# Performance work log

Hardware: AMD Instinct MI355X
Metric: run time of the kernel (lower is better)

The kernel has to match this reference:

```python
import jax, jax.numpy as jnp
import numpy as np

EMB = 1024
HEADS = 16
HEAD_DIM = EMB // HEADS


def setup_inputs() -> dict:
    key = jax.random.key(0)
    ks = jax.random.split(key, 6)
    B, T, D = 4, 2048, EMB
    s = 1.0 / np.sqrt(D)
    return {
        "x": jax.random.normal(ks[0], (B, T, D), dtype=jnp.float32),
        "Wq": jax.random.normal(ks[1], (D, D), dtype=jnp.float32) * s,
        "Wk": jax.random.normal(ks[2], (D, D), dtype=jnp.float32) * s,
        "Wv": jax.random.normal(ks[3], (D, D), dtype=jnp.float32) * s,
        "Wo": jax.random.normal(ks[4], (D, D), dtype=jnp.float32) * s,
        "bo": jax.random.normal(ks[5], (D,), dtype=jnp.float32) * 0.01,
    }


def reference(x, Wq, Wk, Wv, Wo, bo):
    B, T, D = x.shape
    H, Hd = HEADS, HEAD_DIM
    # torch Linear: x @ W.T ; here W stored [out,in]
    def heads(W):
        return (x @ W.T).reshape(B, T, H, Hd).transpose(0, 2, 1, 3)  # [B,H,T,Hd]
    Q, K, V = heads(Wq), heads(Wk), heads(Wv)
    scores = jnp.einsum("bhqd,bhkd->bhqk", Q, K) / np.sqrt(Hd)
    causal = jnp.triu(jnp.ones((T, T), dtype=bool), k=1)
    scores = jnp.where(causal, -jnp.inf, scores)
    weights = jax.nn.softmax(scores, axis=-1)  # dropout rate 0 -> identity
    ctx = jnp.einsum("bhqk,bhkd->bhqd", weights, V)
    ctx = ctx.transpose(0, 2, 1, 3).reshape(B, T, D)
    return ctx @ Wo.T + bo
```

## Files before the change

kernel.cpp:

```cpp
#include <hip/hip_runtime.h>

typedef short bf16x8 __attribute__((ext_vector_type(8)));
typedef float f32x4 __attribute__((ext_vector_type(4)));
typedef unsigned short u16;
typedef unsigned int u32;

__device__ __forceinline__ u16 f2b(float x) {
  union { float f; u32 u; } c; c.f = x;
  u32 r = (c.u + 0x7FFFu + ((c.u >> 16) & 1u)) >> 16;
  return (u16)r;
}

__device__ __forceinline__ float fexp2(float x) {
  return __builtin_amdgcn_exp2f(x);
}

__device__ __forceinline__ void glds16(const void* g, void* l) {
  __builtin_amdgcn_global_load_lds(
      (const __attribute__((address_space(1))) u32*)g,
      (__attribute__((address_space(3))) u32*)l, 16, 0, 0);
}

__global__ void cvt_kernel(const float* __restrict__ src, u16* __restrict__ dst,
                           int n4, float scale) {
  int i = blockIdx.x * blockDim.x + threadIdx.x;
  if (i >= n4) return;
  float4 v = reinterpret_cast<const float4*>(src)[i];
  ushort4 o;
  o.x = f2b(v.x * scale); o.y = f2b(v.y * scale);
  o.z = f2b(v.z * scale); o.w = f2b(v.w * scale);
  reinterpret_cast<ushort4*>(dst)[i] = o;
}

template<int MODE>
__global__ __launch_bounds__(512, 2)
void gemm2(const u16* __restrict__ A, const u16* __restrict__ Bm,
           u16* __restrict__ Cq, u16* __restrict__ Ck, u16* __restrict__ Cvt,
           float* __restrict__ Cf, const float* __restrict__ bias) {
  constexpr int K = 1024, NKT = K / 64;
  __shared__ __attribute__((aligned(16))) u16 lds[3][24576];
  const int tid = threadIdx.x;
  const int w = tid >> 6;
  const int l = tid & 63;
  const int wm = w >> 2, wn = w & 3;
  const int lr = l & 15, lg = l >> 4;
  const int brow = blockIdx.x * 128;
  const int bcol = blockIdx.y * 256;
  const int wg = w * 64;

  const u16* Ab = A + (size_t)brow * K;
  const u16* Bb = Bm + (size_t)bcol * K;
  int gA[2], lA[2], gB[4], lB[4];
#pragma unroll
  for (int i = 0; i < 2; ++i) {
    const int q = i * 512 + tid;
    const int r = q >> 3, s = (q & 7) ^ (r & 7);
    gA[i] = r * K + s * 8;
    lA[i] = (i * 512 + wg) * 8;
  }
#pragma unroll
  for (int i = 0; i < 4; ++i) {
    const int q = i * 512 + tid;
    const int r = q >> 3, s = (q & 7) ^ (r & 7);
    gB[i] = r * K + s * 8;
    lB[i] = 8192 + (i * 512 + wg) * 8;
  }

  int aoff[4][2], boff[4][2];
#pragma unroll
  for (int m = 0; m < 4; ++m) {
    const int row = wm * 64 + m * 16 + lr;
#pragma unroll
    for (int kk = 0; kk < 2; ++kk)
      aoff[m][kk] = row * 64 + (((kk * 4 + lg) ^ (row & 7)) * 8);
  }
#pragma unroll
  for (int n = 0; n < 4; ++n) {
    const int row = wn * 64 + n * 16 + lr;
#pragma unroll
    for (int kk = 0; kk < 2; ++kk)
      boff[n][kk] = 8192 + row * 64 + (((kk * 4 + lg) ^ (row & 7)) * 8);
  }

  f32x4 acc[4][4] = {};

#pragma unroll
  for (int i = 0; i < 2; ++i) glds16(Ab + gA[i], &lds[0][lA[i]]);
#pragma unroll
  for (int i = 0; i < 4; ++i) glds16(Bb + gB[i], &lds[0][lB[i]]);
#pragma unroll
  for (int i = 0; i < 2; ++i) glds16(Ab + gA[i] + 64, &lds[1][lA[i]]);
#pragma unroll
  for (int i = 0; i < 4; ++i) glds16(Bb + gB[i] + 64, &lds[1][lB[i]]);
  asm volatile("s_waitcnt vmcnt(6)" ::: "memory");
  asm volatile("s_barrier" ::: "memory");

  int bi = 0;
  for (int kt = 0; kt < NKT; ++kt) {
    const u16* Lb = lds[bi];
    const int bs = (bi + 2 >= 3) ? (bi - 1) : (bi + 2);
    const bool st = (kt + 2 < NKT);
    const int ko = (kt + 2) * 64;

    bf16x8 a[4][2], b01[2][2];
#pragma unroll
    for (int m = 0; m < 4; ++m)
#pragma unroll
      for (int kk = 0; kk < 2; ++kk)
        a[m][kk] = *reinterpret_cast<const bf16x8*>(&Lb[aoff[m][kk]]);
#pragma unroll
    for (int n = 0; n < 2; ++n)
#pragma unroll
      for (int kk = 0; kk < 2; ++kk)
        b01[n][kk] = *reinterpret_cast<const bf16x8*>(&Lb[boff[n][kk]]);
    if (st) {
      glds16(Ab + gA[0] + ko, &lds[bs][lA[0]]);
      glds16(Ab + gA[1] + ko, &lds[bs][lA[1]]);
      glds16(Bb + gB[0] + ko, &lds[bs][lB[0]]);
    }
    asm volatile("s_barrier" ::: "memory");
    asm volatile("s_waitcnt lgkmcnt(0)" ::: "memory");
    __builtin_amdgcn_sched_barrier(0);
    __builtin_amdgcn_s_setprio(1);
#pragma unroll
    for (int m = 0; m < 4; ++m)
#pragma unroll
      for (int n = 0; n < 2; ++n)
#pragma unroll
        for (int kk = 0; kk < 2; ++kk)
          acc[m][n] = __builtin_amdgcn_mfma_f32_16x16x32_bf16(a[m][kk], b01[n][kk], acc[m][n], 0, 0, 0);
    __builtin_amdgcn_s_setprio(0);
    asm volatile("s_barrier" ::: "memory");

    bf16x8 b23[2][2];
#pragma unroll
    for (int n = 0; n < 2; ++n)
#pragma unroll
      for (int kk = 0; kk < 2; ++kk)
        b23[n][kk] = *reinterpret_cast<const bf16x8*>(&Lb[boff[n + 2][kk]]);
    if (st) {
      glds16(Bb + gB[1] + ko, &lds[bs][lB[1]]);
      glds16(Bb + gB[2] + ko, &lds[bs][lB[2]]);
      glds16(Bb + gB[3] + ko, &lds[bs][lB[3]]);
    }
    if (kt + 1 < NKT) {
      if (st) asm volatile("s_waitcnt vmcnt(6)" ::: "memory");
      else    asm volatile("s_waitcnt vmcnt(0)" ::: "memory");
    }
    asm volatile("s_barrier" ::: "memory");
    asm volatile("s_waitcnt lgkmcnt(0)" ::: "memory");
    __builtin_amdgcn_sched_barrier(0);
    __builtin_amdgcn_s_setprio(1);
#pragma unroll
    for (int m = 0; m < 4; ++m)
#pragma unroll
      for (int n = 0; n < 2; ++n)
#pragma unroll
        for (int kk = 0; kk < 2; ++kk)
          acc[m][n + 2] = __builtin_amdgcn_mfma_f32_16x16x32_bf16(a[m][kk], b23[n][kk], acc[m][n + 2], 0, 0, 0);
    __builtin_amdgcn_s_setprio(0);
    asm volatile("s_barrier" ::: "memory");

    bi = (bi + 1 >= 3) ? 0 : bi + 1;
  }

  if (MODE == 0) {
    const int seg = blockIdx.y >> 2;
    const int cbase = (blockIdx.y & 3) * 256;
    if (seg < 2) {
      u16* dst = (seg == 0) ? Cq : Ck;
#pragma unroll
      for (int m = 0; m < 4; ++m) {
        const size_t r = (size_t)(brow + wm * 64 + m * 16 + lg * 4);
#pragma unroll
        for (int n = 0; n < 4; ++n) {
          const int c = cbase + wn * 64 + n * 16 + lr;
#pragma unroll
          for (int j = 0; j < 4; ++j)
            dst[(r + j) * 1024 + c] = f2b(acc[m][n][j]);
        }
      }
    } else {
#pragma unroll
      for (int n = 0; n < 4; ++n) {
        const int c = cbase + wn * 64 + n * 16 + lr;
        const int hh = c >> 6, dd = c & 63;
#pragma unroll
        for (int m = 0; m < 4; ++m) {
          const int r0 = brow + wm * 64 + m * 16 + lg * 4;
#pragma unroll
          for (int j = 0; j < 4; ++j) {
            const int r = r0 + j;
            const int bt = r >> 11, tt = r & 2047;
            Cvt[((size_t)((bt * 16 + hh) * 64 + dd)) * 2048 + tt] = f2b(acc[m][n][j]);
          }
        }
      }
    }
  } else {
#pragma unroll
    for (int m = 0; m < 4; ++m) {
      const size_t r = (size_t)(brow + wm * 64 + m * 16 + lg * 4);
#pragma unroll
      for (int n = 0; n < 4; ++n) {
        const int c = bcol + wn * 64 + n * 16 + lr;
        const float bv = bias[c];
#pragma unroll
        for (int j = 0; j < 4; ++j)
          Cf[(r + j) * 1024 + c] = acc[m][n][j] + bv;
      }
    }
  }
}

__global__ __launch_bounds__(256, 3)
void attn_kernel(const u16* __restrict__ qb, const u16* __restrict__ kb,
                 const u16* __restrict__ vt, u16* __restrict__ ctx) {
  __shared__ __attribute__((aligned(16))) u16 Ks[2][64 * 72];
  __shared__ __attribute__((aligned(16))) u16 Vs[2][64 * 72];
  __shared__ __attribute__((aligned(16))) u16 Ps[4 * 32 * 64];
  const int bid = blockIdx.x;
  const int qt = 15 - (bid >> 6);
  const int bh = bid & 63;
  const int bb = bh >> 4, h = bh & 15;
  const int tid = threadIdx.x, w = tid >> 6, l = tid & 63;
  const int lr = l & 15, lg = l >> 4;
  const int Qw = qt * 128 + w * 32;
  const int kvr = tid >> 3;
  const int kvc = (tid & 7) * 8;

  bf16x8 qf[2][2];
#pragma unroll
  for (int mi = 0; mi < 2; ++mi)
#pragma unroll
    for (int kc = 0; kc < 2; ++kc)
      qf[mi][kc] = *reinterpret_cast<const bf16x8*>(
          &qb[(size_t)(bb * 2048 + Qw + mi * 16 + lr) * 1024 + h * 64 + kc * 32 + lg * 8]);

  f32x4 oacc[2][4] = {};
  float lsum[2][4] = {};

  const int ntiles = 2 * qt + 2;

  bf16x8 kr[2], vr[2];
#pragma unroll
  for (int it = 0; it < 2; ++it) {
    kr[it] = *reinterpret_cast<const bf16x8*>(
        &kb[(size_t)(bb * 2048 + it * 32 + kvr) * 1024 + h * 64 + kvc]);
    vr[it] = *reinterpret_cast<const bf16x8*>(
        &vt[(size_t)(bh * 64 + it * 32 + kvr) * 2048 + kvc]);
  }
#pragma unroll
  for (int it = 0; it < 2; ++it) {
    *reinterpret_cast<bf16x8*>(&Ks[0][(it * 32 + kvr) * 72 + kvc]) = kr[it];
    *reinterpret_cast<bf16x8*>(&Vs[0][(it * 32 + kvr) * 72 + kvc]) = vr[it];
  }
  __syncthreads();
#pragma unroll
  for (int it = 0; it < 2; ++it) {
    kr[it] = *reinterpret_cast<const bf16x8*>(
        &kb[(size_t)(bb * 2048 + 64 + it * 32 + kvr) * 1024 + h * 64 + kvc]);
    vr[it] = *reinterpret_cast<const bf16x8*>(
        &vt[(size_t)(bh * 64 + it * 32 + kvr) * 2048 + 64 + kvc]);
  }

  for (int t = 0; t < ntiles; ++t) {
    const int c0 = t * 64;
    const int cur = t & 1;

    if (c0 < Qw + 32) {
      const bool diag = (c0 + 63 > Qw);

      f32x4 sacc[2][4] = {};
      __builtin_amdgcn_s_setprio(1);
#pragma unroll
      for (int kc = 0; kc < 2; ++kc)
#pragma unroll
        for (int nj = 0; nj < 4; ++nj) {
          bf16x8 kf = *reinterpret_cast<const bf16x8*>(
              &Ks[cur][(nj * 16 + lr) * 72 + kc * 32 + lg * 8]);
#pragma unroll
          for (int mi = 0; mi < 2; ++mi)
            sacc[mi][nj] = __builtin_amdgcn_mfma_f32_16x16x32_bf16(qf[mi][kc], kf, sacc[mi][nj], 0, 0, 0);
        }
      __builtin_amdgcn_s_setprio(0);

#pragma unroll
      for (int mi = 0; mi < 2; ++mi) {
        if (diag) {
#pragma unroll
          for (int nj = 0; nj < 4; ++nj) {
            const int col = c0 + nj * 16 + lr;
#pragma unroll
            for (int j = 0; j < 4; ++j) {
              const int row = Qw + mi * 16 + lg * 4 + j;
              if (col > row) sacc[mi][nj][j] = -1e30f;
            }
          }
        }
#pragma unroll
        for (int nj = 0; nj < 4; ++nj) {
          const int cchunk = nj * 2 + (lr >> 3);
          const int coff = lr & 7;
#pragma unroll
          for (int j = 0; j < 4; ++j) {
            const float p = fexp2(sacc[mi][nj][j]);
            lsum[mi][j] += p;
            const int rowP = mi * 16 + lg * 4 + j;
            Ps[w * 2048 + rowP * 64 + ((cchunk ^ (rowP & 7)) * 8) + coff] = f2b(p);
          }
        }
      }

      __builtin_amdgcn_s_setprio(1);
#pragma unroll
      for (int kc = 0; kc < 2; ++kc) {
        bf16x8 pf[2];
#pragma unroll
        for (int mi = 0; mi < 2; ++mi) {
          const int rowP = mi * 16 + lr;
          const int cj = kc * 4 + lg;
          pf[mi] = *reinterpret_cast<const bf16x8*>(
              &Ps[w * 2048 + rowP * 64 + ((cj ^ (rowP & 7)) * 8)]);
        }
#pragma unroll
        for (int nd = 0; nd < 4; ++nd) {
          bf16x8 vf = *reinterpret_cast<const bf16x8*>(
              &Vs[cur][(nd * 16 + lr) * 72 + kc * 32 + lg * 8]);
#pragma unroll
          for (int mi = 0; mi < 2; ++mi)
            oacc[mi][nd] = __builtin_amdgcn_mfma_f32_16x16x32_bf16(pf[mi], vf, oacc[mi][nd], 0, 0, 0);
        }
      }
      __builtin_amdgcn_s_setprio(0);
    }

    if (t + 1 < ntiles) {
#pragma unroll
      for (int it = 0; it < 2; ++it) {
        *reinterpret_cast<bf16x8*>(&Ks[cur ^ 1][(it * 32 + kvr) * 72 + kvc]) = kr[it];
        *reinterpret_cast<bf16x8*>(&Vs[cur ^ 1][(it * 32 + kvr) * 72 + kvc]) = vr[it];
      }
    }
    __syncthreads();
    if (t + 2 < ntiles) {
      const int c0n = c0 + 128;
#pragma unroll
      for (int it = 0; it < 2; ++it) {
        kr[it] = *reinterpret_cast<const bf16x8*>(
            &kb[(size_t)(bb * 2048 + c0n + it * 32 + kvr) * 1024 + h * 64 + kvc]);
        vr[it] = *reinterpret_cast<const bf16x8*>(
            &vt[(size_t)(bh * 64 + it * 32 + kvr) * 2048 + c0n + kvc]);
      }
    }
  }

#pragma unroll
  for (int mi = 0; mi < 2; ++mi) {
#pragma unroll
    for (int x = 1; x < 16; x <<= 1)
#pragma unroll
      for (int j = 0; j < 4; ++j) lsum[mi][j] += __shfl_xor(lsum[mi][j], x, 64);
#pragma unroll
    for (int j = 0; j < 4; ++j) {
      const float inv = 1.0f / lsum[mi][j];
      const size_t r = (size_t)(bb * 2048 + Qw + mi * 16 + lg * 4 + j);
#pragma unroll
      for (int nd = 0; nd < 4; ++nd)
        ctx[r * 1024 + h * 64 + nd * 16 + lr] = f2b(oacc[mi][nd][j] * inv);
    }
  }
}

extern "C" void kernel_launch(void* const* d_in, const int* in_sizes, int n_in,
                              void* d_out, int out_size, void* d_ws, size_t ws_size,
                              hipStream_t stream) {
  const float* x = (const float*)d_in[0];
  const float* Wq = (const float*)d_in[1];
  const float* Wk = (const float*)d_in[2];
  const float* Wv = (const float*)d_in[3];
  const float* Wo = (const float*)d_in[4];
  const float* bo = (const float*)d_in[5];
  float* out = (float*)d_out;

  char* ws = (char*)d_ws;
  u16* xb = (u16*)(ws);
  u16* qb = (u16*)(ws + (16u << 20));
  u16* kb = (u16*)(ws + (32u << 20));
  u16* vtb = (u16*)(ws + (64u << 20));
  u16* wqkvb = (u16*)(ws + (80u << 20));
  u16* wob = (u16*)(ws + (88u << 20));

  const float qscale = 0.125f * 1.4426950408889634f;
  cvt_kernel<<<8192, 256, 0, stream>>>(x, xb, 8388608 / 4, 1.0f);
  cvt_kernel<<<1024, 256, 0, stream>>>(Wq, wqkvb, 1048576 / 4, qscale);
  cvt_kernel<<<1024, 256, 0, stream>>>(Wk, wqkvb + 1048576, 1048576 / 4, 1.0f);
  cvt_kernel<<<1024, 256, 0, stream>>>(Wv, wqkvb + 2097152, 1048576 / 4, 1.0f);
  cvt_kernel<<<1024, 256, 0, stream>>>(Wo, wob, 1048576 / 4, 1.0f);

  gemm2<0><<<dim3(64, 12), 512, 0, stream>>>(xb, wqkvb, qb, kb, vtb, nullptr, nullptr);
  attn_kernel<<<1024, 256, 0, stream>>>(qb, kb, vtb, xb);
  gemm2<1><<<dim3(64, 4), 512, 0, stream>>>(xb, wob, nullptr, nullptr, nullptr, out, bo);
}
```

Measured before the change: 166.4 us.

## Restructure GEMM to 4 waves with 64x128 warp tiles and fuse conversion kernels

The projection GEMMs now run 256-thread blocks with 4 waves, each owning a 64x128 output sub-tile (32 accumulators). The K-step shrinks to 32 with a 3-stage LDS ring using a 4-way XOR swizzle, and the split half-iteration barrier scheme is dropped. The five fp32-to-bf16 conversion launches are merged into one kernel that selects source and scale by index. This aims for more register-level reuse per LDS read and fewer launches, at the cost of higher register pressure, twice as many loop iterations, and fewer waves to hide latency.

```diff
diff --git a/kernel.cpp b/kernel.cpp
--- a/kernel.cpp
+++ b/kernel.cpp
@@ -21,146 +21,114 @@
       (__attribute__((address_space(3))) u32*)l, 16, 0, 0);
 }
 
-__global__ void cvt_kernel(const float* __restrict__ src, u16* __restrict__ dst,
-                           int n4, float scale) {
-  int i = blockIdx.x * blockDim.x + threadIdx.x;
-  if (i >= n4) return;
-  float4 v = reinterpret_cast<const float4*>(src)[i];
+__global__ void cvt_all(const float* __restrict__ x, const float* __restrict__ Wq,
+                        const float* __restrict__ Wk, const float* __restrict__ Wv,
+                        const float* __restrict__ Wo, u16* __restrict__ xb,
+                        u16* __restrict__ wqkvb, u16* __restrict__ wob, float qscale) {
+  const int i = blockIdx.x * blockDim.x + threadIdx.x;
+  const float* src;
+  u16* dst;
+  float scale = 1.0f;
+  int off;
+  if (i < 2097152) {
+    src = x; dst = xb; off = i;
+  } else {
+    const int j = i - 2097152;
+    const int wsel = j >> 18;
+    off = j & 262143;
+    if (wsel == 0)      { src = Wq; dst = wqkvb;            scale = qscale; }
+    else if (wsel == 1) { src = Wk; dst = wqkvb + 1048576; }
+    else if (wsel == 2) { src = Wv; dst = wqkvb + 2097152; }
+    else                { src = Wo; dst = wob; }
+  }
+  float4 v = reinterpret_cast<const float4*>(src)[off];
   ushort4 o;
   o.x = f2b(v.x * scale); o.y = f2b(v.y * scale);
   o.z = f2b(v.z * scale); o.w = f2b(v.w * scale);
-  reinterpret_cast<ushort4*>(dst)[i] = o;
+  reinterpret_cast<ushort4*>(dst)[off] = o;
 }
 
 template<int MODE>
-__global__ __launch_bounds__(512, 2)
+__global__ __launch_bounds__(256, 2)
 void gemm2(const u16* __restrict__ A, const u16* __restrict__ Bm,
            u16* __restrict__ Cq, u16* __restrict__ Ck, u16* __restrict__ Cvt,
            float* __restrict__ Cf, const float* __restrict__ bias) {
-  constexpr int K = 1024, NKT = K / 64;
-  __shared__ __attribute__((aligned(16))) u16 lds[3][24576];
+  constexpr int K = 1024, NKT = 32;
+  __shared__ __attribute__((aligned(16))) u16 lds[3][12288];
   const int tid = threadIdx.x;
-  const int w = tid >> 6;
-  const int l = tid & 63;
-  const int wm = w >> 2, wn = w & 3;
+  const int w = tid >> 6, l = tid & 63;
+  const int wm = w >> 1, wn = w & 1;
   const int lr = l & 15, lg = l >> 4;
   const int brow = blockIdx.x * 128;
   const int bcol = blockIdx.y * 256;
-  const int wg = w * 64;
-
   const u16* Ab = A + (size_t)brow * K;
   const u16* Bb = Bm + (size_t)bcol * K;
-  int gA[2], lA[2], gB[4], lB[4];
+
+  int gA[2], gB[4];
 #pragma unroll
   for (int i = 0; i < 2; ++i) {
-    const int q = i * 512 + tid;
-    const int r = q >> 3, s = (q & 7) ^ (r & 7);
-    gA[i] = r * K + s * 8;
-    lA[i] = (i * 512 + wg) * 8;
+    const int q = i * 256 + tid, r = q >> 2, s = q & 3;
+    gA[i] = r * K + ((s ^ (r & 3)) * 8);
   }
 #pragma unroll
   for (int i = 0; i < 4; ++i) {
-    const int q = i * 512 + tid;
-    const int r = q >> 3, s = (q & 7) ^ (r & 7);
-    gB[i] = r * K + s * 8;
-    lB[i] = 8192 + (i * 512 + wg) * 8;
-  }
-
-  int aoff[4][2], boff[4][2];
+    const int q = i * 256 + tid, r = q >> 2, s = q & 3;
+    gB[i] = r * K + ((s ^ (r & 3)) * 8);
+  }
+  const int ldsw = w * 512;
+
+  int a_off[4], b_off[8];
 #pragma unroll
   for (int m = 0; m < 4; ++m) {
     const int row = wm * 64 + m * 16 + lr;
-#pragma unroll
-    for (int kk = 0; kk < 2; ++kk)
-      aoff[m][kk] = row * 64 + (((kk * 4 + lg) ^ (row & 7)) * 8);
-  }
-#pragma unroll
-  for (int n = 0; n < 4; ++n) {
-    const int row = wn * 64 + n * 16 + lr;
-#pragma unroll
-    for (int kk = 0; kk < 2; ++kk)
-      boff[n][kk] = 8192 + row * 64 + (((kk * 4 + lg) ^ (row & 7)) * 8);
-  }
-
-  f32x4 acc[4][4] = {};
-
-#pragma unroll
-  for (int i = 0; i < 2; ++i) glds16(Ab + gA[i], &lds[0][lA[i]]);
-#pragma unroll
-  for (int i = 0; i < 4; ++i) glds16(Bb + gB[i], &lds[0][lB[i]]);
-#pragma unroll
-  for (int i = 0; i < 2; ++i) glds16(Ab + gA[i] + 64, &lds[1][lA[i]]);
-#pragma unroll
-  for (int i = 0; i < 4; ++i) glds16(Bb + gB[i] + 64, &lds[1][lB[i]]);
+    a_off[m] = (row * 4 + (lg ^ (lr & 3))) * 8;
+  }
+#pragma unroll
+  for (int n = 0; n < 8; ++n) {
+    const int row = wn * 128 + n * 16 + lr;
+    b_off[n] = 4096 + (row * 4 + (lg ^ (lr & 3))) * 8;
+  }
+
+  f32x4 acc[4][8] = {};
+
+#pragma unroll
+  for (int t = 0; t < 2; ++t) {
+#pragma unroll
+    for (int i = 0; i < 2; ++i) glds16(Ab + gA[i] + t * 32, &lds[t][i * 2048 + ldsw]);
+#pragma unroll
+    for (int i = 0; i < 4; ++i) glds16(Bb + gB[i] + t * 32, &lds[t][4096 + i * 2048 + ldsw]);
+  }
   asm volatile("s_waitcnt vmcnt(6)" ::: "memory");
   asm volatile("s_barrier" ::: "memory");
 
   int bi = 0;
   for (int kt = 0; kt < NKT; ++kt) {
     const u16* Lb = lds[bi];
-    const int bs = (bi + 2 >= 3) ? (bi - 1) : (bi + 2);
-    const bool st = (kt + 2 < NKT);
-    const int ko = (kt + 2) * 64;
-
-    bf16x8 a[4][2], b01[2][2];
+    bf16x8 a[4], b[8];
+#pragma unroll
+    for (int m = 0; m < 4; ++m) a[m] = *reinterpret_cast<const bf16x8*>(&Lb[a_off[m]]);
+#pragma unroll
+    for (int n = 0; n < 8; ++n) b[n] = *reinterpret_cast<const bf16x8*>(&Lb[b_off[n]]);
+    if (kt + 2 < NKT) {
+      const int bs = (bi + 2 >= 3) ? (bi - 1) : (bi + 2);
+      const int ko = (kt + 2) * 32;
+#pragma unroll
+      for (int i = 0; i < 2; ++i) glds16(Ab + gA[i] + ko, &lds[bs][i * 2048 + ldsw]);
+#pragma unroll
+      for (int i = 0; i < 4; ++i) glds16(Bb + gB[i] + ko, &lds[bs][4096 + i * 2048 + ldsw]);
+    }
+    __builtin_amdgcn_s_setprio(1);
 #pragma unroll
     for (int m = 0; m < 4; ++m)
 #pragma unroll
-      for (int kk = 0; kk < 2; ++kk)
-        a[m][kk] = *reinterpret_cast<const bf16x8*>(&Lb[aoff[m][kk]]);
-#pragma unroll
-    for (int n = 0; n < 2; ++n)
-#pragma unroll
-      for (int kk = 0; kk < 2; ++kk)
-        b01[n][kk] = *reinterpret_cast<const bf16x8*>(&Lb[boff[n][kk]]);
-    if (st) {
-      glds16(Ab + gA[0] + ko, &lds[bs][lA[0]]);
-      glds16(Ab + gA[1] + ko, &lds[bs][lA[1]]);
-      glds16(Bb + gB[0] + ko, &lds[bs][lB[0]]);
+      for (int n = 0; n < 8; ++n)
+        acc[m][n] = __builtin_amdgcn_mfma_f32_16x16x32_bf16(a[m], b[n], acc[m][n], 0, 0, 0);
+    __builtin_amdgcn_s_setprio(0);
+    if (kt + 1 < NKT) {
+      if (kt + 2 < NKT) asm volatile("s_waitcnt vmcnt(6)" ::: "memory");
+      else              asm volatile("s_waitcnt vmcnt(0)" ::: "memory");
     }
     asm volatile("s_barrier" ::: "memory");
-    asm volatile("s_waitcnt lgkmcnt(0)" ::: "memory");
-    __builtin_amdgcn_sched_barrier(0);
-    __builtin_amdgcn_s_setprio(1);
-#pragma unroll
-    for (int m = 0; m < 4; ++m)
-#pragma unroll
-      for (int n = 0; n < 2; ++n)
-#pragma unroll
-        for (int kk = 0; kk < 2; ++kk)
-          acc[m][n] = __builtin_amdgcn_mfma_f32_16x16x32_bf16(a[m][kk], b01[n][kk], acc[m][n], 0, 0, 0);
-    __builtin_amdgcn_s_setprio(0);
-    asm volatile("s_barrier" ::: "memory");
-
-    bf16x8 b23[2][2];
-#pragma unroll
-    for (int n = 0; n < 2; ++n)
-#pragma unroll
-      for (int kk = 0; kk < 2; ++kk)
-        b23[n][kk] = *reinterpret_cast<const bf16x8*>(&Lb[boff[n + 2][kk]]);
-    if (st) {
-      glds16(Bb + gB[1] + ko, &lds[bs][lB[1]]);
-      glds16(Bb + gB[2] + ko, &lds[bs][lB[2]]);
-      glds16(Bb + gB[3] + ko, &lds[bs][lB[3]]);
-    }
-    if (kt + 1 < NKT) {
-      if (st) asm volatile("s_waitcnt vmcnt(6)" ::: "memory");
-      else    asm volatile("s_waitcnt vmcnt(0)" ::: "memory");
-    }
-    asm volatile("s_barrier" ::: "memory");
-    asm volatile("s_waitcnt lgkmcnt(0)" ::: "memory");
-    __builtin_amdgcn_sched_barrier(0);
-    __builtin_amdgcn_s_setprio(1);
-#pragma unroll
-    for (int m = 0; m < 4; ++m)
-#pragma unroll
-      for (int n = 0; n < 2; ++n)
-#pragma unroll
-        for (int kk = 0; kk < 2; ++kk)
-          acc[m][n + 2] = __builtin_amdgcn_mfma_f32_16x16x32_bf16(a[m][kk], b23[n][kk], acc[m][n + 2], 0, 0, 0);
-    __builtin_amdgcn_s_setprio(0);
-    asm volatile("s_barrier" ::: "memory");
-
     bi = (bi + 1 >= 3) ? 0 : bi + 1;
   }
 
@@ -171,19 +139,19 @@
       u16* dst = (seg == 0) ? Cq : Ck;
 #pragma unroll
       for (int m = 0; m < 4; ++m) {
-        const size_t r = (size_t)(brow + wm * 64 + m * 16 + lg * 4);
-#pragma unroll
-        for (int n = 0; n < 4; ++n) {
-          const int c = cbase + wn * 64 + n * 16 + lr;
+        const size_t r0 = (size_t)(brow + wm * 64 + m * 16 + lg * 4);
+#pragma unroll
+        for (int n = 0; n < 8; ++n) {
+          const int c = cbase + wn * 128 + n * 16 + lr;
 #pragma unroll
           for (int j = 0; j < 4; ++j)
-            dst[(r + j) * 1024 + c] = f2b(acc[m][n][j]);
+            dst[(r0 + j) * 1024 + c] = f2b(acc[m][n][j]);
         }
       }
     } else {
 #pragma unroll
-      for (int n = 0; n < 4; ++n) {
-        const int c = cbase + wn * 64 + n * 16 + lr;
+      for (int n = 0; n < 8; ++n) {
+        const int c = cbase + wn * 128 + n * 16 + lr;
         const int hh = c >> 6, dd = c & 63;
 #pragma unroll
         for (int m = 0; m < 4; ++m) {
@@ -200,14 +168,14 @@
   } else {
 #pragma unroll
     for (int m = 0; m < 4; ++m) {
-      const size_t r = (size_t)(brow + wm * 64 + m * 16 + lg * 4);
-#pragma unroll
-      for (int n = 0; n < 4; ++n) {
-        const int c = bcol + wn * 64 + n * 16 + lr;
+      const size_t r0 = (size_t)(brow + wm * 64 + m * 16 + lg * 4);
+#pragma unroll
+      for (int n = 0; n < 8; ++n) {
+        const int c = bcol + wn * 128 + n * 16 + lr;
         const float bv = bias[c];
 #pragma unroll
         for (int j = 0; j < 4; ++j)
-          Cf[(r + j) * 1024 + c] = acc[m][n][j] + bv;
+          Cf[(r0 + j) * 1024 + c] = acc[m][n][j] + bv;
       }
     }
   }
@@ -392,13 +360,9 @@
   u16* wob = (u16*)(ws + (88u << 20));
 
   const float qscale = 0.125f * 1.4426950408889634f;
-  cvt_kernel<<<8192, 256, 0, stream>>>(x, xb, 8388608 / 4, 1.0f);
-  cvt_kernel<<<1024, 256, 0, stream>>>(Wq, wqkvb, 1048576 / 4, qscale);
-  cvt_kernel<<<1024, 256, 0, stream>>>(Wk, wqkvb + 1048576, 1048576 / 4, 1.0f);
-  cvt_kernel<<<1024, 256, 0, stream>>>(Wv, wqkvb + 2097152, 1048576 / 4, 1.0f);
-  cvt_kernel<<<1024, 256, 0, stream>>>(Wo, wob, 1048576 / 4, 1.0f);
-
-  gemm2<0><<<dim3(64, 12), 512, 0, stream>>>(xb, wqkvb, qb, kb, vtb, nullptr, nullptr);
+  cvt_all<<<12288, 256, 0, stream>>>(x, Wq, Wk, Wv, Wo, xb, wqkvb, wob, qscale);
+
+  gemm2<0><<<dim3(64, 12), 256, 0, stream>>>(xb, wqkvb, qb, kb, vtb, nullptr, nullptr);
   attn_kernel<<<1024, 256, 0, stream>>>(qb, kb, vtb, xb);
-  gemm2<1><<<dim3(64, 4), 512, 0, stream>>>(xb, wob, nullptr, nullptr, nullptr, out, bo);
-}
+  gemm2<1><<<dim3(64, 4), 256, 0, stream>>>(xb, wob, nullptr, nullptr, nullptr, out, bo);
+}
```

Result: faster. 157.8 us (-5.1%).

## Widen attention blocks to 256 queries, swizzle K/V LDS, fuse conversion kernels

Applied to the files above, without the earlier changes.

The attention kernel now runs 512-thread blocks, each covering 256 query rows over 8 waves, so every K/V tile staged in LDS is reused by twice as many waves. Padded K/V rows are replaced by an XOR-swizzled layout. Query tiles are ordered so the heaviest causal blocks go first, followed by the lighter ones. The five fp32-to-bf16 conversion launches are merged into a single kernel to cut launch overhead. In exchange, there are half as many blocks and more registers and LDS per block, which could lower occupancy and worsen causal load balance.

```diff
diff --git a/kernel.cpp b/kernel.cpp
--- a/kernel.cpp
+++ b/kernel.cpp
@@ -21,15 +21,31 @@
       (__attribute__((address_space(3))) u32*)l, 16, 0, 0);
 }
 
-__global__ void cvt_kernel(const float* __restrict__ src, u16* __restrict__ dst,
-                           int n4, float scale) {
-  int i = blockIdx.x * blockDim.x + threadIdx.x;
-  if (i >= n4) return;
-  float4 v = reinterpret_cast<const float4*>(src)[i];
+__global__ void cvt_all(const float* __restrict__ x, const float* __restrict__ Wq,
+                        const float* __restrict__ Wk, const float* __restrict__ Wv,
+                        const float* __restrict__ Wo, u16* __restrict__ xb,
+                        u16* __restrict__ wqkvb, u16* __restrict__ wob, float qscale) {
+  const int i = blockIdx.x * blockDim.x + threadIdx.x;
+  const float* src;
+  u16* dst;
+  float scale = 1.0f;
+  int off;
+  if (i < 2097152) {
+    src = x; dst = xb; off = i;
+  } else {
+    const int j = i - 2097152;
+    const int wsel = j >> 18;
+    off = j & 262143;
+    if (wsel == 0)      { src = Wq; dst = wqkvb;            scale = qscale; }
+    else if (wsel == 1) { src = Wk; dst = wqkvb + 1048576; }
+    else if (wsel == 2) { src = Wv; dst = wqkvb + 2097152; }
+    else                { src = Wo; dst = wob; }
+  }
+  float4 v = reinterpret_cast<const float4*>(src)[off];
   ushort4 o;
   o.x = f2b(v.x * scale); o.y = f2b(v.y * scale);
   o.z = f2b(v.z * scale); o.w = f2b(v.w * scale);
-  reinterpret_cast<ushort4*>(dst)[i] = o;
+  reinterpret_cast<ushort4*>(dst)[off] = o;
 }
 
 template<int MODE>
@@ -213,21 +229,28 @@
   }
 }
 
-__global__ __launch_bounds__(256, 3)
+__global__ __launch_bounds__(512, 2)
 void attn_kernel(const u16* __restrict__ qb, const u16* __restrict__ kb,
                  const u16* __restrict__ vt, u16* __restrict__ ctx) {
-  __shared__ __attribute__((aligned(16))) u16 Ks[2][64 * 72];
-  __shared__ __attribute__((aligned(16))) u16 Vs[2][64 * 72];
-  __shared__ __attribute__((aligned(16))) u16 Ps[4 * 32 * 64];
+  __shared__ __attribute__((aligned(16))) u16 Ks[2][4096];
+  __shared__ __attribute__((aligned(16))) u16 Vs[2][4096];
+  __shared__ __attribute__((aligned(16))) u16 Ps[8 * 2048];
   const int bid = blockIdx.x;
-  const int qt = 15 - (bid >> 6);
+  const int chunk = bid >> 6;
+  const int qt = (chunk < 4) ? (7 - chunk) : (chunk - 4);
   const int bh = bid & 63;
   const int bb = bh >> 4, h = bh & 15;
   const int tid = threadIdx.x, w = tid >> 6, l = tid & 63;
   const int lr = l & 15, lg = l >> 4;
-  const int Qw = qt * 128 + w * 32;
+  const int Qw = qt * 256 + w * 32;
   const int kvr = tid >> 3;
-  const int kvc = (tid & 7) * 8;
+  const int gv = tid & 7;
+  const int kvc = gv * 8;
+  const int pgW = ((gv ^ (kvr & 7)) * 8);
+
+  int prd[2];
+#pragma unroll
+  for (int kc = 0; kc < 2; ++kc) prd[kc] = ((kc * 4 + lg) ^ (lr & 7)) * 8;
 
   bf16x8 qf[2][2];
 #pragma unroll
@@ -240,29 +263,16 @@
   f32x4 oacc[2][4] = {};
   float lsum[2][4] = {};
 
-  const int ntiles = 2 * qt + 2;
-
-  bf16x8 kr[2], vr[2];
-#pragma unroll
-  for (int it = 0; it < 2; ++it) {
-    kr[it] = *reinterpret_cast<const bf16x8*>(
-        &kb[(size_t)(bb * 2048 + it * 32 + kvr) * 1024 + h * 64 + kvc]);
-    vr[it] = *reinterpret_cast<const bf16x8*>(
-        &vt[(size_t)(bh * 64 + it * 32 + kvr) * 2048 + kvc]);
-  }
-#pragma unroll
-  for (int it = 0; it < 2; ++it) {
-    *reinterpret_cast<bf16x8*>(&Ks[0][(it * 32 + kvr) * 72 + kvc]) = kr[it];
-    *reinterpret_cast<bf16x8*>(&Vs[0][(it * 32 + kvr) * 72 + kvc]) = vr[it];
-  }
+  const int ntiles = 4 * qt + 4;
+
+  bf16x8 kr, vr;
+  kr = *reinterpret_cast<const bf16x8*>(&kb[(size_t)(bb * 2048 + kvr) * 1024 + h * 64 + kvc]);
+  vr = *reinterpret_cast<const bf16x8*>(&vt[(size_t)(bh * 64 + kvr) * 2048 + kvc]);
+  *reinterpret_cast<bf16x8*>(&Ks[0][kvr * 64 + pgW]) = kr;
+  *reinterpret_cast<bf16x8*>(&Vs[0][kvr * 64 + pgW]) = vr;
   __syncthreads();
-#pragma unroll
-  for (int it = 0; it < 2; ++it) {
-    kr[it] = *reinterpret_cast<const bf16x8*>(
-        &kb[(size_t)(bb * 2048 + 64 + it * 32 + kvr) * 1024 + h * 64 + kvc]);
-    vr[it] = *reinterpret_cast<const bf16x8*>(
-        &vt[(size_t)(bh * 64 + it * 32 + kvr) * 2048 + 64 + kvc]);
-  }
+  kr = *reinterpret_cast<const bf16x8*>(&kb[(size_t)(bb * 2048 + 64 + kvr) * 1024 + h * 64 + kvc]);
+  vr = *reinterpret_cast<const bf16x8*>(&vt[(size_t)(bh * 64 + kvr) * 2048 + 64 + kvc]);
 
   for (int t = 0; t < ntiles; ++t) {
     const int c0 = t * 64;
@@ -278,7 +288,7 @@
 #pragma unroll
         for (int nj = 0; nj < 4; ++nj) {
           bf16x8 kf = *reinterpret_cast<const bf16x8*>(
-              &Ks[cur][(nj * 16 + lr) * 72 + kc * 32 + lg * 8]);
+              &Ks[cur][(nj * 16 + lr) * 64 + prd[kc]]);
 #pragma unroll
           for (int mi = 0; mi < 2; ++mi)
             sacc[mi][nj] = __builtin_amdgcn_mfma_f32_16x16x32_bf16(qf[mi][kc], kf, sacc[mi][nj], 0, 0, 0);
@@ -326,7 +336,7 @@
 #pragma unroll
         for (int nd = 0; nd < 4; ++nd) {
           bf16x8 vf = *reinterpret_cast<const bf16x8*>(
-              &Vs[cur][(nd * 16 + lr) * 72 + kc * 32 + lg * 8]);
+              &Vs[cur][(nd * 16 + lr) * 64 + prd[kc]]);
 #pragma unroll
           for (int mi = 0; mi < 2; ++mi)
             oacc[mi][nd] = __builtin_amdgcn_mfma_f32_16x16x32_bf16(pf[mi], vf, oacc[mi][nd], 0, 0, 0);
@@ -336,22 +346,16 @@
     }
 
     if (t + 1 < ntiles) {
-#pragma unroll
-      for (int it = 0; it < 2; ++it) {
-        *reinterpret_cast<bf16x8*>(&Ks[cur ^ 1][(it * 32 + kvr) * 72 + kvc]) = kr[it];
-        *reinterpret_cast<bf16x8*>(&Vs[cur ^ 1][(it * 32 + kvr) * 72 + kvc]) = vr[it];
-      }
+      *reinterpret_cast<bf16x8*>(&Ks[cur ^ 1][kvr * 64 + pgW]) = kr;
+      *reinterpret_cast<bf16x8*>(&Vs[cur ^ 1][kvr * 64 + pgW]) = vr;
     }
     __syncthreads();
     if (t + 2 < ntiles) {
       const int c0n = c0 + 128;
-#pragma unroll
-      for (int it = 0; it < 2; ++it) {
-        kr[it] = *reinterpret_cast<const bf16x8*>(
-            &kb[(size_t)(bb * 2048 + c0n + it * 32 + kvr) * 1024 + h * 64 + kvc]);
-        vr[it] = *reinterpret_cast<const bf16x8*>(
-            &vt[(size_t)(bh * 64 + it * 32 + kvr) * 2048 + c0n + kvc]);
-      }
+      kr = *reinterpret_cast<const bf16x8*>(
+          &kb[(size_t)(bb * 2048 + c0n + kvr) * 1024 + h * 64 + kvc]);
+      vr = *reinterpret_cast<const bf16x8*>(
+          &vt[(size_t)(bh * 64 + kvr) * 2048 + c0n + kvc]);
     }
   }
 
@@ -392,13 +396,9 @@
   u16* wob = (u16*)(ws + (88u << 20));
 
   const float qscale = 0.125f * 1.4426950408889634f;
-  cvt_kernel<<<8192, 256, 0, stream>>>(x, xb, 8388608 / 4, 1.0f);
-  cvt_kernel<<<1024, 256, 0, stream>>>(Wq, wqkvb, 1048576 / 4, qscale);
-  cvt_kernel<<<1024, 256, 0, stream>>>(Wk, wqkvb + 1048576, 1048576 / 4, 1.0f);
-  cvt_kernel<<<1024, 256, 0, stream>>>(Wv, wqkvb + 2097152, 1048576 / 4, 1.0f);
-  cvt_kernel<<<1024, 256, 0, stream>>>(Wo, wob, 1048576 / 4, 1.0f);
+  cvt_all<<<12288, 256, 0, stream>>>(x, Wq, Wk, Wv, Wo, xb, wqkvb, wob, qscale);
 
   gemm2<0><<<dim3(64, 12), 512, 0, stream>>>(xb, wqkvb, qb, kb, vtb, nullptr, nullptr);
-  attn_kernel<<<1024, 256, 0, stream>>>(qb, kb, vtb, xb);
+  attn_kernel<<<512, 512, 0, stream>>>(qb, kb, vtb, xb);
   gemm2<1><<<dim3(64, 4), 512, 0, stream>>>(xb, wob, nullptr, nullptr, nullptr, out, bo);
 }
```

Result: slower. 172.5 us (+3.7%).
